# Kernel optimization log

Hardware: AMD Instinct MI355X
Metric: run time of the kernel (lower is better)

Reference implementation:

```python
import jax, jax.numpy as jnp
import numpy as np

B, S = 64, 512
NUM_C = 1000
SKILL_DIM = ANSWER_DIM = HIDDEN = 256
ATTN_DIM = 80
LSTM_IN = SKILL_DIM + ANSWER_DIM  # 512


def setup_inputs() -> dict:
    key = jax.random.key(0)
    ks = jax.random.split(key, 12)
    sc = 0.05
    return {
        "skill": jax.random.randint(ks[0], (B, S), 0, NUM_C),
        "answer": jax.random.randint(ks[1], (B, S), 0, 2),
        "skill_emb": jax.random.normal(ks[2], (NUM_C + 1, SKILL_DIM), jnp.float32) * sc,
        "answer_emb": jax.random.normal(ks[3], (3, ANSWER_DIM), jnp.float32) * sc,
        "Wih": jax.random.normal(ks[4], (4 * HIDDEN, LSTM_IN), jnp.float32) * sc,
        "Whh": jax.random.normal(ks[5], (4 * HIDDEN, HIDDEN), jnp.float32) * sc,
        "bih": jnp.zeros((4 * HIDDEN,), jnp.float32),
        "bhh": jnp.zeros((4 * HIDDEN,), jnp.float32),
        "mlp_W": jax.random.normal(ks[6], (ATTN_DIM, HIDDEN), jnp.float32) * sc,
        "mlp_b": jnp.zeros((ATTN_DIM,), jnp.float32),
        "sim_W": jax.random.normal(ks[7], (1, ATTN_DIM), jnp.float32) * sc,
        "fc_W": jax.random.normal(ks[8], (NUM_C, 2 * HIDDEN), jnp.float32) * sc,
        "fc_b": jnp.zeros((NUM_C,), jnp.float32),
    }


def _lstm(x, Wih, Whh, bih, bhh):
    # x: [B, S, In] -> h_seq: [B, S, H]. PyTorch gate order: i, f, g, o.
    Bsz = x.shape[0]
    H = Whh.shape[1]
    x_t = jnp.swapaxes(x, 0, 1)  # [S, B, In]
    xproj = x_t @ Wih.T + (bih + bhh)  # precompute input projection [S, B, 4H]

    def step(carry, xp):
        h, c = carry
        gates = xp + h @ Whh.T
        i, f, g, o = jnp.split(gates, 4, axis=-1)
        i, f, o = jax.nn.sigmoid(i), jax.nn.sigmoid(f), jax.nn.sigmoid(o)
        g = jnp.tanh(g)
        c = f * c + i * g
        h = o * jnp.tanh(c)
        return (h, c), h

    init = (jnp.zeros((Bsz, H), x.dtype), jnp.zeros((Bsz, H), x.dtype))
    _, hs = jax.lax.scan(step, init, xproj)
    return jnp.swapaxes(hs, 0, 1)  # [B, S, H]


def reference(skill, answer, skill_emb, answer_emb, Wih, Whh, bih, bhh,
              mlp_W, mlp_b, sim_W, fc_W, fc_b):
    se = skill_emb[skill]    # [B, S, Ds]
    ae = answer_emb[answer]  # [B, S, Da]
    skill_answer = jnp.concatenate([se, ae], axis=2)
    answer_skill = jnp.concatenate([ae, se], axis=2)
    cond = (answer == 1)[:, :, None]
    sa_emb = jnp.where(cond, skill_answer, answer_skill)  # [B, S, In]

    out = _lstm(sa_emb, Wih, Whh, bih, bhh)  # [B, S, H]

    # attention_module (fix=True path)
    att = jnp.tanh(out @ mlp_W.T + mlp_b) @ sim_W.T  # [B, S, 1]
    att = att[:, :, 0]  # [B, S] (score of each key position)
    seq = att.shape[1]
    # causal mask: position i attends to j <= i; strictly-upper entries -> -inf
    mask = jnp.triu(jnp.ones((seq, seq), bool), k=1)
    scores = jnp.where(mask[None, :, :], -jnp.inf, att[:, None, :])  # [B, S, S]
    alphas = jax.nn.softmax(scores, axis=-1)
    attn_out = jnp.einsum('bij,bjh->bih', alphas, out)  # [B, S, H]
    attn_cum_1 = jnp.cumsum(attn_out, axis=1) - attn_out
    final = jnp.concatenate([attn_cum_1, out], axis=2)  # [B, S, 2H]

    res = jax.nn.sigmoid(final @ fc_W.T + fc_b)  # [B, S, num_c]
    return res, sa_emb
```

## Files before the change

### kernel.cpp

```cpp
#include <hip/hip_runtime.h>


typedef _Float16 half8 __attribute__((ext_vector_type(8)));
typedef _Float16 half4 __attribute__((ext_vector_type(4)));
typedef float f32x4 __attribute__((ext_vector_type(4)));

#define BS 32768
#define NC 1000

__device__ __forceinline__ float sigm(float x) {
    return __builtin_amdgcn_rcpf(1.f + __expf(-x));
}
__device__ __forceinline__ float tanh_(float x) {
    float e = __expf(2.f * x);
    return 1.f - 2.f * __builtin_amdgcn_rcpf(e + 1.f);
}

__global__ void prep_kernel(const float* __restrict__ Wih, const float* __restrict__ fcW,
                            const float* __restrict__ mlpW, const float* __restrict__ se,
                            const float* __restrict__ ae, const float* __restrict__ bih,
                            const float* __restrict__ bhh,
                            _Float16* __restrict__ wih16, _Float16* __restrict__ fcw16,
                            _Float16* __restrict__ mlpw16, _Float16* __restrict__ se16,
                            float* __restrict__ bsum, float* __restrict__ qvec) {
    int i = blockIdx.x * 256 + threadIdx.x;
    if (i < 524288) {
        wih16[i] = (_Float16)Wih[i];
    } else if (i < 1048576) {
        int j = i - 524288;
        int r = j >> 9;
        fcw16[j] = (r < NC) ? (_Float16)fcW[j] : (_Float16)0.f;
    } else if (i < 1081344) {
        int j = i - 1048576;
        int r = j >> 8;
        mlpw16[j] = (r < 80) ? (_Float16)mlpW[j] : (_Float16)0.f;
    } else if (i < 1337600) {
        int j = i - 1081344;
        se16[j] = (_Float16)se[j];
    } else if (i < 1338624) {
        int j = i - 1337600;
        bsum[j] = bih[j] + bhh[j];
    } else if (i < 1340672) {
        int j = i - 1338624;
        int which = j >> 10, col = j & 1023;
        int aerow = (which == 0) ? 1 : 0;
        int koff  = (which == 0) ? 256 : 0;
        float s = 0.f;
        for (int k = 0; k < 256; k++)
            s += ae[aerow * 256 + k] * Wih[(size_t)col * 512 + koff + k];
        qvec[j] = s + bih[col] + bhh[col];
    }
}

__global__ void embed_kernel(const int* __restrict__ skill, const int* __restrict__ answer,
                             const float* __restrict__ se, const float* __restrict__ ae,
                             float* __restrict__ sa_out, int* __restrict__ ridx) {
    int token = blockIdx.x;
    int sk = skill[token], an = answer[token];
    const float* first  = (an == 1) ? (se + (size_t)sk * 256) : (ae + (size_t)an * 256);
    const float* second = (an == 1) ? (ae + (size_t)an * 256) : (se + (size_t)sk * 256);
    int j = threadIdx.x * 4;
    const float* src = (j < 256) ? (first + j) : (second + (j - 256));
    float4 v = *(const float4*)src;
    *(float4*)(sa_out + (size_t)token * 512 + j) = v;
    if (threadIdx.x == 0) ridx[token] = (an == 1) ? sk : (1024 + sk);
}

__global__ __launch_bounds__(256) void tgemm_kernel(
        const _Float16* __restrict__ A, const _Float16* __restrict__ Bw,
        const float* __restrict__ qvec, _Float16* __restrict__ Tsw) {
    int bm = blockIdx.x * 128, bn = blockIdx.y * 128;
    int which = bm >> 10;
    int mbase = bm & 1023;
    int koff = which ? 256 : 0;
    int tid = threadIdx.x, wv = tid >> 6, lane = tid & 63;
    int quad = lane >> 4, l16 = lane & 15;
    int wm = (wv & 1) * 64, wn = (wv >> 1) * 64;

    int arow[4];
#pragma unroll
    for (int i = 0; i < 4; i++) {
        int r = mbase + wm + i * 16 + l16;
        arow[i] = (r > 1000) ? 1000 : r;
    }
    const _Float16* Bbase = Bw + (size_t)(bn + wn + l16) * 512 + koff + quad * 8;

    f32x4 acc[4][4] = {};
    for (int kk = 0; kk < 256; kk += 32) {
        half8 a[4], b[4];
#pragma unroll
        for (int i = 0; i < 4; i++)
            a[i] = *(const half8*)(A + (size_t)arow[i] * 256 + quad * 8 + kk);
#pragma unroll
        for (int j = 0; j < 4; j++)
            b[j] = *(const half8*)(Bbase + (size_t)j * 16 * 512 + kk);
#pragma unroll
        for (int i = 0; i < 4; i++)
#pragma unroll
            for (int j = 0; j < 4; j++)
                acc[i][j] = __builtin_amdgcn_mfma_f32_16x16x32_f16(a[i], b[j], acc[i][j], 0, 0, 0);
    }
#pragma unroll
    for (int j = 0; j < 4; j++) {
        int col = bn + wn + j * 16 + l16;
        float qv = qvec[which * 1024 + col];
        int perm = ((col & 255) >> 5) * 128 + (((col >> 4) & 1)) * 64 + (col & 15) * 4 + (col >> 8);
#pragma unroll
        for (int i = 0; i < 4; i++) {
            int row = mbase + wm + i * 16 + quad * 4;
#pragma unroll
            for (int r = 0; r < 4; r++) {
                if (row + r > 1000) continue;
                Tsw[(size_t)((which << 10) + row + r) * 1024 + perm] = (_Float16)(acc[i][j][r] + qv);
            }
        }
    }
}

__global__ __launch_bounds__(512, 2) void lstm_kernel(
        const float* __restrict__ Whh,
        const _Float16* __restrict__ Tsw,
        const int* __restrict__ ridxArr,
        _Float16* __restrict__ outH) {
    int bid = blockIdx.x;
    int tid = threadIdx.x, wv = tid >> 6, lane = tid & 63;
    int quad = lane >> 4, l16 = lane & 15;
    int row = lane >> 5;
    int hc  = lane & 31;
    int pr = hc >> 4, hcLow = hc & 15;

    extern __shared__ char smem[];
    _Float16* ldsB = (_Float16*)smem;
    float*    rd   = (float*)(smem + 133152);

    half8 rB[48];
#pragma unroll
    for (int v = 0; v < 8; v++) {
#pragma unroll
        for (int k = 0; k < 8; k++) {
            int col = (v >> 1) * 256 + wv * 32 + (v & 1) * 16 + l16;
            const float* p = Whh + (size_t)col * 256 + k * 32 + quad * 8;
            float4 x0 = *(const float4*)p;
            float4 x1 = *(const float4*)(p + 4);
            half8 hb;
            hb[0] = (_Float16)x0.x; hb[1] = (_Float16)x0.y; hb[2] = (_Float16)x0.z; hb[3] = (_Float16)x0.w;
            hb[4] = (_Float16)x1.x; hb[5] = (_Float16)x1.y; hb[6] = (_Float16)x1.z; hb[7] = (_Float16)x1.w;
            if (k < 6) rB[k * 8 + v] = hb;
            else *(half8*)(ldsB + ((size_t)wv * 16 + (k - 6) * 8 + v) * 512 + lane * 8) = hb;
        }
    }
    if (tid < 130) ((float4*)(smem + 131072))[tid] = float4{0.f, 0.f, 0.f, 0.f};

    int b0 = bid * 2 + row;
    int tb = b0 * 512;
    _Float16* po = outH + (size_t)b0 * 512 * 256 + wv * 32 + hc;

    bool realA = (l16 < 2);
    int hb0 = realA ? (131072 + l16 * 512 + quad * 16) : 133120;
    int hb1 = realA ? (131072 + 1024 + l16 * 512 + quad * 16) : 133120;
    int kstep = realA ? 64 : 0;

    float c = 0.f;
    half4 Tcur;
    unsigned ridxA;
    {
        int r0 = ridxArr[tb];
        Tcur = *(const half4*)(Tsw + (size_t)r0 * 1024 + wv * 128 + pr * 64 + hcLow * 4);
        ridxA = ridxArr[tb + 1];
    }
    __syncthreads();

    int cur = 0;
    for (int t = 0; t < 512; t++) {
        int tn2 = (t + 2 < 512) ? t + 2 : 511;
        half4 Tnx = *(const half4*)(Tsw + (size_t)ridxA * 1024 + wv * 128 + pr * 64 + hcLow * 4);
        unsigned ridxB = ridxArr[tb + tn2];

        f32x4 acc[8];
#pragma unroll
        for (int v = 0; v < 8; v++) acc[v] = f32x4{0.f, 0.f, 0.f, 0.f};

        const char* hp = smem + (cur ? hb1 : hb0);
#pragma unroll
        for (int k = 0; k < 8; k++) {
            half8 av = *(const half8*)hp;
            hp += kstep;
#pragma unroll
            for (int v = 0; v < 8; v++) {
                half8 bv;
                if (k < 6) bv = rB[k * 8 + v];
                else bv = *(const half8*)(ldsB + ((size_t)wv * 16 + (k - 6) * 8 + v) * 512 + lane * 8);
                acc[v] = __builtin_amdgcn_mfma_f32_16x16x32_f16(av, bv, acc[v], 0, 0, 0);
            }
        }

        if (quad == 0) {
#pragma unroll
            for (int r2 = 0; r2 < 2; r2++)
#pragma unroll
                for (int par = 0; par < 2; par++) {
                    f32x4 pv;
                    pv[0] = acc[0 + par][r2];
                    pv[1] = acc[2 + par][r2];
                    pv[2] = acc[4 + par][r2];
                    pv[3] = acc[6 + par][r2];
                    *(f32x4*)(rd + wv * 256 + (par * 32 + r2 * 16 + l16) * 4) = pv;
                }
        }
        f32x4 pa = *(const f32x4*)(rd + wv * 256 + (pr * 32 + row * 16 + hcLow) * 4);

        float ii = sigm(pa[0] + (float)Tcur[0]);
        float ff = sigm(pa[1] + (float)Tcur[1]);
        float gg = tanh_(pa[2] + (float)Tcur[2]);
        float oo = sigm(pa[3] + (float)Tcur[3]);
        c = ff * c + ii * gg;
        float h = oo * tanh_(c);
        _Float16 hf = (_Float16)h;

        *(_Float16*)(smem + 131072 + ((cur ^ 1) << 10) + (row << 9) + (wv * 32 + hc) * 2) = hf;

        __syncthreads();
        cur ^= 1;

        po[0] = hf;
        po += 256;
        Tcur = Tnx;
        ridxA = ridxB;
    }
}

__global__ __launch_bounds__(256) void gemm_f16(
        const _Float16* __restrict__ A, const _Float16* __restrict__ Bw,
        const float* __restrict__ bias, float* __restrict__ C,
        int K, int ldC, int Nstore, int epi) {
    int bm = blockIdx.x * 128, bn = blockIdx.y * 128;
    int tid = threadIdx.x, wv = tid >> 6, lane = tid & 63;
    int quad = lane >> 4, l16 = lane & 15;
    int wm = (wv & 1) * 64, wn = (wv >> 1) * 64;

    const _Float16* Abase = A + (size_t)(bm + wm + l16) * K + quad * 8;
    const _Float16* Bbase = Bw + (size_t)(bn + wn + l16) * K + quad * 8;

    f32x4 acc[4][4] = {};
    for (int kk = 0; kk < K; kk += 32) {
        half8 a[4], b[4];
#pragma unroll
        for (int i = 0; i < 4; i++) a[i] = *(const half8*)(Abase + (size_t)i * 16 * K + kk);
#pragma unroll
        for (int j = 0; j < 4; j++) b[j] = *(const half8*)(Bbase + (size_t)j * 16 * K + kk);
#pragma unroll
        for (int i = 0; i < 4; i++)
#pragma unroll
            for (int j = 0; j < 4; j++)
                acc[i][j] = __builtin_amdgcn_mfma_f32_16x16x32_f16(a[i], b[j], acc[i][j], 0, 0, 0);
    }
#pragma unroll
    for (int j = 0; j < 4; j++) {
        int col = bn + wn + j * 16 + l16;
        if (col >= Nstore) continue;
        float bv = bias ? bias[col] : 0.f;
#pragma unroll
        for (int i = 0; i < 4; i++) {
            int row0 = bm + wm + i * 16 + quad * 4;
#pragma unroll
            for (int r = 0; r < 4; r++) {
                float v = acc[i][j][r] + bv;
                if (epi == 1) v = sigm(v);
                C[(size_t)(row0 + r) * ldC + col] = v;
            }
        }
    }
}

__global__ void att_kernel(const float* __restrict__ mlpout, const float* __restrict__ simW,
                           float* __restrict__ att) {
    int m = blockIdx.x * 256 + threadIdx.x;
    float s = 0.f;
#pragma unroll
    for (int d = 0; d < 80; d += 4) {
        float4 v = *(const float4*)(mlpout + (size_t)m * 80 + d);
        float4 w = *(const float4*)(simW + d);
        s += tanh_(v.x) * w.x + tanh_(v.y) * w.y + tanh_(v.z) * w.z + tanh_(v.w) * w.w;
    }
    att[m] = s;
}

__global__ __launch_bounds__(256) void scan_kernel(const float* __restrict__ att,
                                                   const _Float16* __restrict__ outH,
                                                   _Float16* __restrict__ finalB) {
    int b = blockIdx.x, d = threadIdx.x;
    __shared__ float w_s[512];
    for (int i = d; i < 512; i += 256) w_s[i] = __expf(att[(size_t)b * 512 + i]);
    __syncthreads();

    float S = 0.f, W = 0.f, C = 0.f;
    const _Float16* op = outH + (size_t)b * 512 * 256 + d;
    _Float16* fp = finalB + (size_t)b * 512 * 512 + d;
    for (int i = 0; i < 512; i++) {
        float w = w_s[i];
        float ov = (float)op[(size_t)i * 256];
        S += w * ov;
        W += w;
        float ao = S * __builtin_amdgcn_rcpf(W);
        fp[(size_t)i * 512]       = (_Float16)C;
        fp[(size_t)i * 512 + 256] = (_Float16)ov;
        C += ao;
    }
}

extern "C" void kernel_launch(void* const* d_in, const int* in_sizes, int n_in,
                              void* d_out, int out_size, void* d_ws, size_t ws_size,
                              hipStream_t stream) {
    const int*   skill      = (const int*)d_in[0];
    const int*   answer     = (const int*)d_in[1];
    const float* skill_emb  = (const float*)d_in[2];
    const float* answer_emb = (const float*)d_in[3];
    const float* Wih        = (const float*)d_in[4];
    const float* Whh        = (const float*)d_in[5];
    const float* bih        = (const float*)d_in[6];
    const float* bhh        = (const float*)d_in[7];
    const float* mlp_W      = (const float*)d_in[8];
    const float* mlp_b      = (const float*)d_in[9];
    const float* sim_W      = (const float*)d_in[10];
    const float* fc_W       = (const float*)d_in[11];
    const float* fc_b       = (const float*)d_in[12];

    float* res    = (float*)d_out;
    float* sa_out = res + (size_t)BS * NC;

    char* ws = (char*)d_ws;
    _Float16* outH   = (_Float16*)(ws);
    _Float16* finalB = (_Float16*)(ws + 16777216);
    _Float16* wih16  = (_Float16*)(ws + 50331648);
    _Float16* fcw16  = (_Float16*)(ws + 51380224);
    _Float16* mlpw16 = (_Float16*)(ws + 52428800);
    _Float16* se16   = (_Float16*)(ws + 52494336);
    float*    bsum   = (float*)(ws + 53018624);
    float*    qvec   = (float*)(ws + 53022720);
    float*    att    = (float*)(ws + 53030912);
    float*    mlpout = (float*)(ws + 53161984);
    _Float16* Tsw    = (_Float16*)(ws + 63647744);
    int*      ridx   = (int*)(ws + 67842048);

    (void)bsum; (void)in_sizes; (void)n_in; (void)out_size; (void)ws_size;

    hipLaunchKernelGGL(prep_kernel, dim3(5238), dim3(256), 0, stream,
                       Wih, fc_W, mlp_W, skill_emb, answer_emb, bih, bhh,
                       wih16, fcw16, mlpw16, se16, bsum, qvec);
    hipLaunchKernelGGL(embed_kernel, dim3(BS), dim3(128), 0, stream,
                       skill, answer, skill_emb, answer_emb, sa_out, ridx);
    hipLaunchKernelGGL(tgemm_kernel, dim3(16, 8), dim3(256), 0, stream,
                       se16, wih16, qvec, Tsw);

    hipFuncSetAttribute((const void*)lstm_kernel,
                        hipFuncAttributeMaxDynamicSharedMemorySize, 141344);
    hipLaunchKernelGGL(lstm_kernel, dim3(32), dim3(512), 141344, stream,
                       Whh, Tsw, ridx, outH);

    hipLaunchKernelGGL(gemm_f16, dim3(256, 1), dim3(256), 0, stream,
                       outH, mlpw16, mlp_b, mlpout, 256, 80, 80, 0);
    hipLaunchKernelGGL(att_kernel, dim3(128), dim3(256), 0, stream, mlpout, sim_W, att);
    hipLaunchKernelGGL(scan_kernel, dim3(64), dim3(256), 0, stream, att, outH, finalB);
    hipLaunchKernelGGL(gemm_f16, dim3(256, 8), dim3(256), 0, stream,
                       finalB, fcw16, fc_b, res, 512, 1000, 1000, 1);
}
```

Before: 1.369 ms.

## Stream half of recurrent weights from global/L2 instead of LDS and registers

The LSTM kernel now keeps only the first four K-slices of Whh in registers and drops the 128KB LDS copy of the last two slices. Slices 4-7 are pre-swizzled into a fp16 global buffer by prep_kernel and reloaded from global/L2 every timestep, double-buffered so the loads overlap the MFMAs. This cuts register pressure and LDS footprint, but adds per-step global load latency on the serial recurrence path.

```diff
diff --git a/kernel.cpp b/kernel.cpp
--- a/kernel.cpp
+++ b/kernel.cpp
@@ -19,10 +19,11 @@
 __global__ void prep_kernel(const float* __restrict__ Wih, const float* __restrict__ fcW,
                             const float* __restrict__ mlpW, const float* __restrict__ se,
                             const float* __restrict__ ae, const float* __restrict__ bih,
-                            const float* __restrict__ bhh,
+                            const float* __restrict__ bhh, const float* __restrict__ Whh,
                             _Float16* __restrict__ wih16, _Float16* __restrict__ fcw16,
                             _Float16* __restrict__ mlpw16, _Float16* __restrict__ se16,
-                            float* __restrict__ bsum, float* __restrict__ qvec) {
+                            float* __restrict__ bsum, float* __restrict__ qvec,
+                            _Float16* __restrict__ gwhh16) {
     int i = blockIdx.x * 256 + threadIdx.x;
     if (i < 524288) {
         wih16[i] = (_Float16)Wih[i];
@@ -49,6 +50,15 @@
         for (int k = 0; k < 256; k++)
             s += ae[aerow * 256 + k] * Wih[(size_t)col * 512 + koff + k];
         qvec[j] = s + bih[col] + bhh[col];
+    } else if (i < 1471744) {
+        int j = i - 1340672;
+        int fi = j >> 9;
+        int r  = j & 511;
+        int lane = r >> 3, e = r & 7;
+        int wv = fi >> 5, kg = (fi >> 3) & 3, v = fi & 7;
+        int col  = (v >> 1) * 256 + wv * 32 + (v & 1) * 16 + (lane & 15);
+        int krow = (4 + kg) * 32 + (lane >> 4) * 8 + e;
+        gwhh16[j] = (_Float16)Whh[(size_t)col * 256 + krow];
     }
 }
 
@@ -117,10 +127,22 @@
     }
 }
 
+#define LSTM_K(kk, BV) { \
+    half8 av = *(const half8*)(smem + (realA ? (hb + (kk) * 64) : (2112 - ((kk) & 1) * 64))); \
+    _Pragma("unroll") \
+    for (int v = 0; v < 8; v++) \
+        acc[v] = __builtin_amdgcn_mfma_f32_16x16x32_f16(av, BV, acc[v], 0, 0, 0); }
+
+#define LOAD_G(dst, kg) { \
+    _Pragma("unroll") \
+    for (int v = 0; v < 8; v++) \
+        dst[v] = *(const half8*)(gw + ((kg) * 8 + v) * 512); }
+
 __global__ __launch_bounds__(512, 2) void lstm_kernel(
         const float* __restrict__ Whh,
         const _Float16* __restrict__ Tsw,
         const int* __restrict__ ridxArr,
+        const _Float16* __restrict__ gwhh,
         _Float16* __restrict__ outH) {
     int bid = blockIdx.x;
     int tid = threadIdx.x, wv = tid >> 6, lane = tid & 63;
@@ -129,36 +151,33 @@
     int hc  = lane & 31;
     int pr = hc >> 4, hcLow = hc & 15;
 
-    extern __shared__ char smem[];
-    _Float16* ldsB = (_Float16*)smem;
-    float*    rd   = (float*)(smem + 133152);
-
-    half8 rB[48];
+    __shared__ __align__(16) char smem[10368];
+    float* rd = (float*)(smem + 2176);
+
+    half8 rB[32];
 #pragma unroll
     for (int v = 0; v < 8; v++) {
 #pragma unroll
-        for (int k = 0; k < 8; k++) {
+        for (int k = 0; k < 4; k++) {
             int col = (v >> 1) * 256 + wv * 32 + (v & 1) * 16 + l16;
             const float* p = Whh + (size_t)col * 256 + k * 32 + quad * 8;
             float4 x0 = *(const float4*)p;
             float4 x1 = *(const float4*)(p + 4);
-            half8 hb;
-            hb[0] = (_Float16)x0.x; hb[1] = (_Float16)x0.y; hb[2] = (_Float16)x0.z; hb[3] = (_Float16)x0.w;
-            hb[4] = (_Float16)x1.x; hb[5] = (_Float16)x1.y; hb[6] = (_Float16)x1.z; hb[7] = (_Float16)x1.w;
-            if (k < 6) rB[k * 8 + v] = hb;
-            else *(half8*)(ldsB + ((size_t)wv * 16 + (k - 6) * 8 + v) * 512 + lane * 8) = hb;
+            half8 hb8;
+            hb8[0] = (_Float16)x0.x; hb8[1] = (_Float16)x0.y; hb8[2] = (_Float16)x0.z; hb8[3] = (_Float16)x0.w;
+            hb8[4] = (_Float16)x1.x; hb8[5] = (_Float16)x1.y; hb8[6] = (_Float16)x1.z; hb8[7] = (_Float16)x1.w;
+            rB[k * 8 + v] = hb8;
         }
     }
-    if (tid < 130) ((float4*)(smem + 131072))[tid] = float4{0.f, 0.f, 0.f, 0.f};
+    if (tid < 133) ((float4*)smem)[tid] = float4{0.f, 0.f, 0.f, 0.f};
 
     int b0 = bid * 2 + row;
     int tb = b0 * 512;
     _Float16* po = outH + (size_t)b0 * 512 * 256 + wv * 32 + hc;
 
     bool realA = (l16 < 2);
-    int hb0 = realA ? (131072 + l16 * 512 + quad * 16) : 133120;
-    int hb1 = realA ? (131072 + 1024 + l16 * 512 + quad * 16) : 133120;
-    int kstep = realA ? 64 : 0;
+    int hbB = l16 * 512 + quad * 16;
+    const _Float16* gw = gwhh + (size_t)wv * 16384 + lane * 8;
 
     float c = 0.f;
     half4 Tcur;
@@ -176,23 +195,25 @@
         half4 Tnx = *(const half4*)(Tsw + (size_t)ridxA * 1024 + wv * 128 + pr * 64 + hcLow * 4);
         unsigned ridxB = ridxArr[tb + tn2];
 
+        half8 gA[8], gB[8];
+        LOAD_G(gA, 0);
+        LOAD_G(gB, 1);
+
         f32x4 acc[8];
 #pragma unroll
         for (int v = 0; v < 8; v++) acc[v] = f32x4{0.f, 0.f, 0.f, 0.f};
 
-        const char* hp = smem + (cur ? hb1 : hb0);
-#pragma unroll
-        for (int k = 0; k < 8; k++) {
-            half8 av = *(const half8*)hp;
-            hp += kstep;
-#pragma unroll
-            for (int v = 0; v < 8; v++) {
-                half8 bv;
-                if (k < 6) bv = rB[k * 8 + v];
-                else bv = *(const half8*)(ldsB + ((size_t)wv * 16 + (k - 6) * 8 + v) * 512 + lane * 8);
-                acc[v] = __builtin_amdgcn_mfma_f32_16x16x32_f16(av, bv, acc[v], 0, 0, 0);
-            }
-        }
+        int hb = hbB + cur * 1024;
+        LSTM_K(0, rB[0 * 8 + v]);
+        LSTM_K(1, rB[1 * 8 + v]);
+        LSTM_K(2, rB[2 * 8 + v]);
+        LSTM_K(3, rB[3 * 8 + v]);
+        LSTM_K(4, gA[v]);
+        LOAD_G(gA, 2);
+        LSTM_K(5, gB[v]);
+        LOAD_G(gB, 3);
+        LSTM_K(6, gA[v]);
+        LSTM_K(7, gB[v]);
 
         if (quad == 0) {
 #pragma unroll
@@ -217,7 +238,7 @@
         float h = oo * tanh_(c);
         _Float16 hf = (_Float16)h;
 
-        *(_Float16*)(smem + 131072 + ((cur ^ 1) << 10) + (row << 9) + (wv * 32 + hc) * 2) = hf;
+        *(_Float16*)(smem + ((cur ^ 1) << 10) + (row << 9) + (wv * 32 + hc) * 2) = hf;
 
         __syncthreads();
         cur ^= 1;
@@ -342,20 +363,20 @@
     _Float16* Tsw    = (_Float16*)(ws + 63647744);
     int*      ridx   = (int*)(ws + 67842048);
 
+    _Float16* gwhh = (_Float16*)(ws + 63647744 - 262144);
+
     (void)bsum; (void)in_sizes; (void)n_in; (void)out_size; (void)ws_size;
 
-    hipLaunchKernelGGL(prep_kernel, dim3(5238), dim3(256), 0, stream,
-                       Wih, fc_W, mlp_W, skill_emb, answer_emb, bih, bhh,
-                       wih16, fcw16, mlpw16, se16, bsum, qvec);
+    hipLaunchKernelGGL(prep_kernel, dim3(5749), dim3(256), 0, stream,
+                       Wih, fc_W, mlp_W, skill_emb, answer_emb, bih, bhh, Whh,
+                       wih16, fcw16, mlpw16, se16, bsum, qvec, gwhh);
     hipLaunchKernelGGL(embed_kernel, dim3(BS), dim3(128), 0, stream,
                        skill, answer, skill_emb, answer_emb, sa_out, ridx);
     hipLaunchKernelGGL(tgemm_kernel, dim3(16, 8), dim3(256), 0, stream,
                        se16, wih16, qvec, Tsw);
 
-    hipFuncSetAttribute((const void*)lstm_kernel,
-                        hipFuncAttributeMaxDynamicSharedMemorySize, 141344);
-    hipLaunchKernelGGL(lstm_kernel, dim3(32), dim3(512), 141344, stream,
-                       Whh, Tsw, ridx, outH);
+    hipLaunchKernelGGL(lstm_kernel, dim3(32), dim3(512), 0, stream,
+                       Whh, Tsw, ridx, gwhh, outH);
 
     hipLaunchKernelGGL(gemm_f16, dim3(256, 1), dim3(256), 0, stream,
                        outH, mlpw16, mlp_b, mlpout, 256, 80, 80, 0);
```

Measured after the change: 2.668 ms. +94.9%, slower.
